# Optimization experiments

Hardware: AMD Instinct MI355X
Metric: run time of the kernel (lower is better)

Reference implementation:

```python
import jax, jax.numpy as jnp
import numpy as np


def pnp(contour, h, w):
    """Even-odd point-in-polygon rasterization.
    contour: [P, N, 2] float (x, y) pixel coords -> [P, h, w] float {0,1} masks.
    Scans over the N polygon edges (fixed structural dim), toggling parity.
    """
    P, N, _ = contour.shape
    py = jnp.arange(h, dtype=contour.dtype)[:, None]   # [h, 1]
    px = jnp.arange(w, dtype=contour.dtype)[None, :]   # [1, w]
    verts = jnp.moveaxis(contour, 1, 0)                # [N, P, 2]
    nxt = jnp.roll(verts, -1, axis=0)                  # next vertex per edge

    def step(inside, vn):
        v, n = vn
        x1 = v[:, 0][:, None, None]; y1 = v[:, 1][:, None, None]
        x2 = n[:, 0][:, None, None]; y2 = n[:, 1][:, None, None]
        crosses = (y1 > py) != (y2 > py)               # edge straddles scanline
        denom = jnp.where(y2 == y1, 1.0, y2 - y1)
        xint = (x2 - x1) * (py - y1) / denom + x1      # x of edge at scanline
        hit = crosses & (px < xint)
        return inside ^ hit, None

    inside0 = jnp.zeros((P, h, w), dtype=bool)
    inside, _ = jax.lax.scan(step, inside0, (verts, nxt))
    return inside.astype(jnp.float32)


def setup_inputs() -> dict:
    key = jax.random.key(0)
    k1, k2, k3, k4 = jax.random.split(key, 4)
    bs, c_in, h, w = 8, 64, 256, 256
    P, num_point = 40, 128
    ct_num = jax.random.randint(k1, (bs,), 1, 16)  # at least one contour per image
    cx = jax.random.uniform(k2, (P, num_point), minval=0.0, maxval=float(w - 1))
    cy = jax.random.uniform(k3, (P, num_point), minval=0.0, maxval=float(h - 1))
    contour = jnp.stack([cx, cy], axis=-1)                     # [P, N, 2]
    cnn_feature = jax.random.normal(k4, (bs, c_in, h, w), dtype=jnp.float32)
    return {"contour": contour, "cnn_feature": cnn_feature, "ct_num": ct_num}


def reference(contour, cnn_feature, ct_num):
    bs, c_in, h, w = cnn_feature.shape
    mask = pnp(contour, h, w)                                  # [P, h, w]
    max_channel = int(jnp.max(ct_num))
    # Faithful to original: slice start for batch i>=1 is ct_num[i-1] (not cumsum)
    starts = jnp.concatenate([jnp.zeros((1,), ct_num.dtype), ct_num[:-1]])
    j = jnp.arange(max_channel)
    idx = starts[:, None] + j[None, :]                         # [bs, C]
    valid = j[None, :] < ct_num[:, None]                       # [bs, C]
    gathered = mask[jnp.clip(idx, 0, mask.shape[0] - 1)]       # [bs, C, h, w]
    mask_batch = jnp.where(valid[:, :, None, None], gathered, 0.0)
    max_mask = jnp.max(mask_batch, axis=1, keepdims=True)      # [bs, 1, h, w]
    cnn_out = jax.nn.relu(max_mask * cnn_feature + cnn_feature)
    return mask_batch, cnn_out
```

## Files before the change

kernel.cpp:

```cpp
#include <hip/hip_runtime.h>

#define P_NUM 40
#define N_VERT 128
#define H 256
#define W 256
#define BS 8
#define C_IN 64
#define PIX (H * W)
#define PIX4 (PIX / 4)

__global__ __launch_bounds__(256) void pnp_mask_kernel(
    const float* __restrict__ contour, float* __restrict__ maskws) {
    const int p = blockIdx.x;
    const int y = blockIdx.y;
    const int tid = threadIdx.x;

    __shared__ float sx[N_VERT];
    __shared__ float sy[N_VERT];
    __shared__ float xints[N_VERT];
    __shared__ int kcnt;

    if (tid < N_VERT) {
        const float2 v = reinterpret_cast<const float2*>(contour)[p * N_VERT + tid];
        sx[tid] = v.x;
        sy[tid] = v.y;
    }
    if (tid == 0) kcnt = 0;
    __syncthreads();

    const float py = (float)y;
    if (tid < N_VERT) {
        const float y1 = sy[tid];
        const int e2 = (tid + 1) & (N_VERT - 1);
        const float y2 = sy[e2];
        const bool crosses = (y1 > py) != (y2 > py);
        if (crosses) {
            const float x1 = sx[tid];
            const float x2 = sx[e2];
            const float denom = (y2 == y1) ? 1.0f : (y2 - y1);
            const float xint = (x2 - x1) * (py - y1) / denom + x1;
            const int slot = atomicAdd(&kcnt, 1);
            xints[slot] = xint;
        }
    }
    __syncthreads();

    const int K = kcnt;
    const float px = (float)tid;
    int cnt = 0;
    for (int k = 0; k < K; ++k) {
        cnt += (px < xints[k]) ? 1 : 0;
    }
    maskws[(p * H + y) * W + tid] = (float)(cnt & 1);
}

__global__ __launch_bounds__(256) void gather_fuse_kernel(
    const float* __restrict__ maskws, const float* __restrict__ feat,
    const int* __restrict__ ct_num, float* __restrict__ out_mask,
    float* __restrict__ out_cnn, int C) {
    const int gid = blockIdx.x * blockDim.x + threadIdx.x;
    const int i = gid / PIX4;
    const int q = gid - i * PIX4;

    const int cn = ct_num[i];
    const int start = (i == 0) ? 0 : ct_num[i - 1];

    float4 mx = make_float4(0.f, 0.f, 0.f, 0.f);
    for (int j = 0; j < C; ++j) {
        float4 m = make_float4(0.f, 0.f, 0.f, 0.f);
        if (j < cn) {
            int p = start + j;
            p = min(max(p, 0), P_NUM - 1);
            m = reinterpret_cast<const float4*>(maskws)[p * PIX4 + q];
        }
        reinterpret_cast<float4*>(out_mask)[(size_t)(i * C + j) * PIX4 + q] = m;
        mx.x = fmaxf(mx.x, m.x);
        mx.y = fmaxf(mx.y, m.y);
        mx.z = fmaxf(mx.z, m.z);
        mx.w = fmaxf(mx.w, m.w);
    }

    for (int c = 0; c < C_IN; ++c) {
        const float4 f =
            reinterpret_cast<const float4*>(feat)[(size_t)(i * C_IN + c) * PIX4 + q];
        float4 r;
        r.x = fmaxf(mx.x * f.x + f.x, 0.0f);
        r.y = fmaxf(mx.y * f.y + f.y, 0.0f);
        r.z = fmaxf(mx.z * f.z + f.z, 0.0f);
        r.w = fmaxf(mx.w * f.w + f.w, 0.0f);
        reinterpret_cast<float4*>(out_cnn)[(size_t)(i * C_IN + c) * PIX4 + q] = r;
    }
}

extern "C" void kernel_launch(void* const* d_in, const int* in_sizes, int n_in,
                              void* d_out, int out_size, void* d_ws, size_t ws_size,
                              hipStream_t stream) {
    const float* contour = (const float*)d_in[0];
    const float* feat = (const float*)d_in[1];
    const int* ct_num = (const int*)d_in[2];

    float* out = (float*)d_out;
    const int cnn_elems = BS * C_IN * PIX;
    const int C = (out_size - cnn_elems) / (BS * PIX);

    float* maskws = (float*)d_ws;
    float* out_mask = out;
    float* out_cnn = out + (size_t)BS * C * PIX;

    hipLaunchKernelGGL(pnp_mask_kernel, dim3(P_NUM, H), dim3(256), 0, stream,
                       contour, maskws);

    const int total = BS * PIX4;
    hipLaunchKernelGGL(gather_fuse_kernel, dim3(total / 256), dim3(256), 0, stream,
                       maskws, feat, ct_num, out_mask, out_cnn, C);
}
```

Before: 66.06 us.

## Split gather-max and feature fuse into separate kernels with nontemporal stores

Splits the fused gather/max/relu kernel into a gather+max kernel writing an intermediate max mask and a fully parallel elementwise fuse kernel over batch×channel×pixels. This removes the serial per-thread loop over 64 feature channels that left only 512 blocks of work. Output stores use nontemporal hints to avoid cache pollution. It costs an extra launch and an intermediate buffer round-trip in workspace.

```diff
diff --git a/kernel.cpp b/kernel.cpp
--- a/kernel.cpp
+++ b/kernel.cpp
@@ -7,7 +7,11 @@
 #define BS 8
 #define C_IN 64
 #define PIX (H * W)
+#define PIX2 (PIX / 2)
 #define PIX4 (PIX / 4)
+
+typedef float vf2 __attribute__((ext_vector_type(2)));
+typedef float vf4 __attribute__((ext_vector_type(4)));
 
 __global__ __launch_bounds__(256) void pnp_mask_kernel(
     const float* __restrict__ contour, float* __restrict__ maskws) {
@@ -21,7 +25,7 @@
     __shared__ int kcnt;
 
     if (tid < N_VERT) {
-        const float2 v = reinterpret_cast<const float2*>(contour)[p * N_VERT + tid];
+        const vf2 v = reinterpret_cast<const vf2*>(contour)[p * N_VERT + tid];
         sx[tid] = v.x;
         sy[tid] = v.y;
     }
@@ -54,42 +58,48 @@
     maskws[(p * H + y) * W + tid] = (float)(cnt & 1);
 }
 
-__global__ __launch_bounds__(256) void gather_fuse_kernel(
-    const float* __restrict__ maskws, const float* __restrict__ feat,
-    const int* __restrict__ ct_num, float* __restrict__ out_mask,
-    float* __restrict__ out_cnn, int C) {
+__global__ __launch_bounds__(256) void gather_max_kernel(
+    const float* __restrict__ maskws, const int* __restrict__ ct_num,
+    float* __restrict__ out_mask, float* __restrict__ max_mask, int C) {
     const int gid = blockIdx.x * blockDim.x + threadIdx.x;
-    const int i = gid / PIX4;
-    const int q = gid - i * PIX4;
+    const int i = gid / PIX2;
+    const int q = gid - i * PIX2;
 
     const int cn = ct_num[i];
     const int start = (i == 0) ? 0 : ct_num[i - 1];
 
-    float4 mx = make_float4(0.f, 0.f, 0.f, 0.f);
+    vf2 mx = {0.f, 0.f};
     for (int j = 0; j < C; ++j) {
-        float4 m = make_float4(0.f, 0.f, 0.f, 0.f);
+        vf2 m = {0.f, 0.f};
         if (j < cn) {
-            int p = start + j;
-            p = min(max(p, 0), P_NUM - 1);
-            m = reinterpret_cast<const float4*>(maskws)[p * PIX4 + q];
+            int p = min(max(start + j, 0), P_NUM - 1);
+            m = reinterpret_cast<const vf2*>(maskws)[p * PIX2 + q];
         }
-        reinterpret_cast<float4*>(out_mask)[(size_t)(i * C + j) * PIX4 + q] = m;
+        __builtin_nontemporal_store(
+            m, reinterpret_cast<vf2*>(out_mask) + (size_t)(i * C + j) * PIX2 + q);
         mx.x = fmaxf(mx.x, m.x);
         mx.y = fmaxf(mx.y, m.y);
-        mx.z = fmaxf(mx.z, m.z);
-        mx.w = fmaxf(mx.w, m.w);
     }
+    reinterpret_cast<vf2*>(max_mask)[gid] = mx;
+}
 
-    for (int c = 0; c < C_IN; ++c) {
-        const float4 f =
-            reinterpret_cast<const float4*>(feat)[(size_t)(i * C_IN + c) * PIX4 + q];
-        float4 r;
-        r.x = fmaxf(mx.x * f.x + f.x, 0.0f);
-        r.y = fmaxf(mx.y * f.y + f.y, 0.0f);
-        r.z = fmaxf(mx.z * f.z + f.z, 0.0f);
-        r.w = fmaxf(mx.w * f.w + f.w, 0.0f);
-        reinterpret_cast<float4*>(out_cnn)[(size_t)(i * C_IN + c) * PIX4 + q] = r;
-    }
+__global__ __launch_bounds__(256) void fuse_relu_kernel(
+    const float* __restrict__ feat, const float* __restrict__ max_mask,
+    float* __restrict__ out_cnn) {
+    const int gid = blockIdx.x * blockDim.x + threadIdx.x;
+    const int ic = gid / PIX4;
+    const int q = gid - ic * PIX4;
+    const int i = ic >> 6;
+
+    const vf4 f = reinterpret_cast<const vf4*>(feat)[(size_t)ic * PIX4 + q];
+    const vf4 mm = reinterpret_cast<const vf4*>(max_mask)[i * PIX4 + q];
+    vf4 r;
+    r.x = fmaxf(mm.x * f.x + f.x, 0.0f);
+    r.y = fmaxf(mm.y * f.y + f.y, 0.0f);
+    r.z = fmaxf(mm.z * f.z + f.z, 0.0f);
+    r.w = fmaxf(mm.w * f.w + f.w, 0.0f);
+    __builtin_nontemporal_store(
+        r, reinterpret_cast<vf4*>(out_cnn) + (size_t)ic * PIX4 + q);
 }
 
 extern "C" void kernel_launch(void* const* d_in, const int* in_sizes, int n_in,
@@ -104,13 +114,16 @@
     const int C = (out_size - cnn_elems) / (BS * PIX);
 
     float* maskws = (float*)d_ws;
+    float* max_mask = maskws + (size_t)P_NUM * PIX;
     float* out_mask = out;
     float* out_cnn = out + (size_t)BS * C * PIX;
 
     hipLaunchKernelGGL(pnp_mask_kernel, dim3(P_NUM, H), dim3(256), 0, stream,
                        contour, maskws);
 
-    const int total = BS * PIX4;
-    hipLaunchKernelGGL(gather_fuse_kernel, dim3(total / 256), dim3(256), 0, stream,
-                       maskws, feat, ct_num, out_mask, out_cnn, C);
+    hipLaunchKernelGGL(gather_max_kernel, dim3(BS * PIX2 / 256), dim3(256), 0,
+                       stream, maskws, ct_num, out_mask, max_mask, C);
+
+    hipLaunchKernelGGL(fuse_relu_kernel, dim3(BS * C_IN * PIX4 / 256), dim3(256),
+                       0, stream, feat, max_mask, out_cnn);
 }
```

After: 62.03 us. -6.1%, faster.

## Split feature channels across blocks and use nontemporal stores in fused kernel

Applied to the files above, without the earlier changes.

The gather/fuse kernel now splits the 64 feature channels across four blocks per pixel chunk, giving four times as many blocks to fill the GPU. Each split block recomputes the max mask over only the valid contours, and only split 0 writes the mask_batch output. Outputs are written with nontemporal stores to avoid polluting cache with streaming writes. The cost is redundant mask reads, since each pixel's masks are read by four blocks.

```diff
diff --git a/kernel.cpp b/kernel.cpp
--- a/kernel.cpp
+++ b/kernel.cpp
@@ -8,6 +8,11 @@
 #define C_IN 64
 #define PIX (H * W)
 #define PIX4 (PIX / 4)
+#define CSPLIT 4
+#define CPS (C_IN / CSPLIT)
+
+typedef float vf2 __attribute__((ext_vector_type(2)));
+typedef float vf4 __attribute__((ext_vector_type(4)));
 
 __global__ __launch_bounds__(256) void pnp_mask_kernel(
     const float* __restrict__ contour, float* __restrict__ maskws) {
@@ -21,7 +26,7 @@
     __shared__ int kcnt;
 
     if (tid < N_VERT) {
-        const float2 v = reinterpret_cast<const float2*>(contour)[p * N_VERT + tid];
+        const vf2 v = reinterpret_cast<const vf2*>(contour)[p * N_VERT + tid];
         sx[tid] = v.x;
         sy[tid] = v.y;
     }
@@ -54,41 +59,55 @@
     maskws[(p * H + y) * W + tid] = (float)(cnt & 1);
 }
 
-__global__ __launch_bounds__(256) void gather_fuse_kernel(
+__global__ __launch_bounds__(256) void mega_kernel(
     const float* __restrict__ maskws, const float* __restrict__ feat,
     const int* __restrict__ ct_num, float* __restrict__ out_mask,
     float* __restrict__ out_cnn, int C) {
-    const int gid = blockIdx.x * blockDim.x + threadIdx.x;
-    const int i = gid / PIX4;
-    const int q = gid - i * PIX4;
+    const int bid = blockIdx.x;
+    const int split = bid & (CSPLIT - 1);
+    const int chunk = (bid >> 2) & 63;
+    const int i = bid >> 8;
+    const int qv = chunk * 256 + threadIdx.x;
 
     const int cn = ct_num[i];
     const int start = (i == 0) ? 0 : ct_num[i - 1];
 
-    float4 mx = make_float4(0.f, 0.f, 0.f, 0.f);
-    for (int j = 0; j < C; ++j) {
-        float4 m = make_float4(0.f, 0.f, 0.f, 0.f);
-        if (j < cn) {
-            int p = start + j;
-            p = min(max(p, 0), P_NUM - 1);
-            m = reinterpret_cast<const float4*>(maskws)[p * PIX4 + q];
+    vf4 mx = {0.f, 0.f, 0.f, 0.f};
+    if (split == 0) {
+        for (int j = 0; j < C; ++j) {
+            vf4 m = {0.f, 0.f, 0.f, 0.f};
+            if (j < cn) {
+                const int p = min(max(start + j, 0), P_NUM - 1);
+                m = reinterpret_cast<const vf4*>(maskws)[p * PIX4 + qv];
+                mx.x = fmaxf(mx.x, m.x);
+                mx.y = fmaxf(mx.y, m.y);
+                mx.z = fmaxf(mx.z, m.z);
+                mx.w = fmaxf(mx.w, m.w);
+            }
+            __builtin_nontemporal_store(
+                m, reinterpret_cast<vf4*>(out_mask) + (size_t)(i * C + j) * PIX4 + qv);
         }
-        reinterpret_cast<float4*>(out_mask)[(size_t)(i * C + j) * PIX4 + q] = m;
-        mx.x = fmaxf(mx.x, m.x);
-        mx.y = fmaxf(mx.y, m.y);
-        mx.z = fmaxf(mx.z, m.z);
-        mx.w = fmaxf(mx.w, m.w);
+    } else {
+        for (int j = 0; j < cn; ++j) {
+            const int p = min(max(start + j, 0), P_NUM - 1);
+            const vf4 m = reinterpret_cast<const vf4*>(maskws)[p * PIX4 + qv];
+            mx.x = fmaxf(mx.x, m.x);
+            mx.y = fmaxf(mx.y, m.y);
+            mx.z = fmaxf(mx.z, m.z);
+            mx.w = fmaxf(mx.w, m.w);
+        }
     }
 
-    for (int c = 0; c < C_IN; ++c) {
-        const float4 f =
-            reinterpret_cast<const float4*>(feat)[(size_t)(i * C_IN + c) * PIX4 + q];
-        float4 r;
+    const int cbase = split * CPS;
+    for (int cc = 0; cc < CPS; ++cc) {
+        const size_t idx = (size_t)(i * C_IN + cbase + cc) * PIX4 + qv;
+        const vf4 f = reinterpret_cast<const vf4*>(feat)[idx];
+        vf4 r;
         r.x = fmaxf(mx.x * f.x + f.x, 0.0f);
         r.y = fmaxf(mx.y * f.y + f.y, 0.0f);
         r.z = fmaxf(mx.z * f.z + f.z, 0.0f);
         r.w = fmaxf(mx.w * f.w + f.w, 0.0f);
-        reinterpret_cast<float4*>(out_cnn)[(size_t)(i * C_IN + c) * PIX4 + q] = r;
+        __builtin_nontemporal_store(r, reinterpret_cast<vf4*>(out_cnn) + idx);
     }
 }
 
@@ -110,7 +129,6 @@
     hipLaunchKernelGGL(pnp_mask_kernel, dim3(P_NUM, H), dim3(256), 0, stream,
                        contour, maskws);
 
-    const int total = BS * PIX4;
-    hipLaunchKernelGGL(gather_fuse_kernel, dim3(total / 256), dim3(256), 0, stream,
+    hipLaunchKernelGGL(mega_kernel, dim3(BS * 64 * CSPLIT), dim3(256), 0, stream,
                        maskws, feat, ct_num, out_mask, out_cnn, C);
 }
```

Result: no change. 65.96 us (-0.2%).
